# Kernel tuning notes

Measured on AMD Instinct MI355X. Metric: run time of the kernel, lower is better.

The kernel has to match this reference:

```python
import jax, jax.numpy as jnp
import numpy as np
import math

B, N, C, H = 32, 512, 768, 12
HD = C // H
KEEP_RATE = 0.7
SCALE = HD ** -0.5
BOUNDARY = math.ceil(KEEP_RATE * (N - 1))  # 358


def setup_inputs() -> dict:
    key = jax.random.key(0)
    k1, k2, k3, k4 = jax.random.split(key, 4)
    x = jax.random.normal(k1, (B, N, C), jnp.float32) * 0.02
    # prefix (left-aligned) key-padding mask: valid length per sample in [N//4, N]
    lengths = jax.random.randint(k2, (B,), N // 4, N + 1)
    key_mask = (jnp.arange(N)[None, :] < lengths[:, None])  # [B, N]
    attn_mask = jnp.broadcast_to(key_mask[:, None, :], (B, N, N)).astype(jnp.int32)
    w_qkv = jax.random.normal(k3, (C, 3 * C), jnp.float32) * (C ** -0.5)
    w_proj = jax.random.normal(k4, (C, C), jnp.float32) * (C ** -0.5)
    b_proj = jnp.zeros((C,), jnp.float32)
    return {"x": x, "attn_mask": attn_mask, "w_qkv": w_qkv, "w_proj": w_proj, "b_proj": b_proj}


def reference(x, attn_mask, w_qkv, w_proj, b_proj):
    # qkv projection and head split: [B,N,3C] -> [3,B,H,N,HD]
    qkv = (x @ w_qkv).reshape(B, N, 3, H, HD).transpose(2, 0, 3, 1, 4)
    q, k, v = qkv[0], qkv[1], qkv[2]
    attn = jnp.einsum('bhqd,bhkd->bhqk', q, k) * SCALE          # [B,H,N,N]
    mask4 = attn_mask[:, None, :, :]                            # broadcast over heads
    attn = jnp.where(mask4 == 0, jnp.float32(-1e9), attn)
    attn = jax.nn.softmax(attn, axis=-1)
    out = jnp.einsum('bhqk,bhkd->bhqd', attn, v)                # [B,H,N,HD]
    out = out.transpose(0, 2, 1, 3).reshape(B, N, C)
    out = out @ w_proj + b_proj

    # per-sample top-k token pruning based on CLS attention (keep_rate < 1)
    key_row = attn_mask[:, 0, 1:]                               # [B, N-1] key padding row
    cls_mean = attn[:, :, 0, 1:].mean(axis=1)                   # mean over heads, [B, N-1]
    valid = key_row != 0
    scores = jnp.where(valid, cls_mean, -jnp.inf)
    valid_count = valid.sum(axis=1)                             # [B]
    left = jnp.ceil(valid_count.astype(jnp.float32) * KEEP_RATE).astype(jnp.int32)
    _, top_idx = jax.lax.top_k(scores, BOUNDARY)                # sorted desc, [B, BOUNDARY]
    pos = jnp.arange(BOUNDARY)[None, :]
    # slots beyond per-sample left_tokens are padded with 1e9 (matches torch cat padding)
    idx = jnp.where(pos < left[:, None], top_idx.astype(jnp.float32), jnp.float32(1e9))
    index = jnp.broadcast_to(idx[:, :, None], (B, BOUNDARY, C))
    return (out, index, idx, BOUNDARY)
```

## Files before the change

### kernel.cpp

```cpp
#include <hip/hip_runtime.h>

#define Bb 32
#define Nn 512
#define Cc 768
#define Hh 12
#define HDd 64
#define BND 358
#define SCL 0.125f

typedef unsigned short u16;
typedef unsigned int u32;
typedef __attribute__((ext_vector_type(8))) short bf16x8;
typedef __attribute__((ext_vector_type(4))) float f32x4;
typedef __attribute__((ext_vector_type(4))) int i32x4;

__device__ __forceinline__ f32x4 MFMA16(bf16x8 a, bf16x8 b, f32x4 c) {
  return __builtin_amdgcn_mfma_f32_16x16x32_bf16(a, b, c, 0, 0, 0);
}

__device__ __forceinline__ u32 f2bf(float f) {
  u32 u = __builtin_bit_cast(u32, f);
  return (u + 0x7fffu + ((u >> 16) & 1u)) >> 16;
}
__device__ __forceinline__ u32 packbf2(float a, float b) { return f2bf(a) | (f2bf(b) << 16); }
__device__ __forceinline__ float bf2f(u16 h) { return __builtin_bit_cast(float, (u32)h << 16); }

__device__ __forceinline__ void async_copy16(void* lds, const void* g) {
  __builtin_amdgcn_global_load_lds((const __attribute__((address_space(1))) void*)g,
                                   (__attribute__((address_space(3))) void*)lds, 16, 0, 0);
}


__global__ __launch_bounds__(256) void k_convx(const float* __restrict__ x, u16* __restrict__ xb) {
  int gid = blockIdx.x * 256 + threadIdx.x;
  if (gid >= (Bb * Nn * Cc) / 4) return;
  float4 v = *(const float4*)&x[gid * 4];
  u32 p0 = packbf2(v.x, v.y), p1 = packbf2(v.z, v.w);
  uint2 st = {p0, p1};
  *(uint2*)&xb[gid * 4] = st;
}

__global__ __launch_bounds__(256) void k_transpose(const float* __restrict__ src, u16* __restrict__ dst,
                                                   int R, int Ccols) {
  __shared__ float tbuf[32][33];
  int c0 = blockIdx.x * 32, r0 = blockIdx.y * 32;
  int lx = threadIdx.x & 31, ly = threadIdx.x >> 5;
  #pragma unroll
  for (int rr = ly; rr < 32; rr += 8) tbuf[rr][lx] = src[(long)(r0 + rr) * Ccols + c0 + lx];
  __syncthreads();
  #pragma unroll
  for (int cc = ly; cc < 32; cc += 8) dst[(long)(c0 + cc) * R + r0 + lx] = (u16)f2bf(tbuf[lx][cc]);
}

__global__ __launch_bounds__(256) void k_lens(const int* __restrict__ mask, int* __restrict__ lens) {
  int b = blockIdx.x, t = threadIdx.x;
  __shared__ int red[256];
  red[t] = mask[(long)b * Nn * Nn + t] + mask[(long)b * Nn * Nn + t + 256];
  __syncthreads();
  for (int s = 128; s > 0; s >>= 1) {
    if (t < s) red[t] += red[t + s];
    __syncthreads();
  }
  if (t == 0) lens[b] = red[0];
}

template <int MODE, int SWAP>
__global__ __launch_bounds__(256) void k_gemm2(const u16* __restrict__ A, const u16* __restrict__ Bt,
                                               int nb0, u16* __restrict__ Qo, u16* __restrict__ Ko,
                                               u16* __restrict__ Vto, float* __restrict__ Co,
                                               const float* __restrict__ bias) {
  __shared__ u16 As[2][128 * 64];
  __shared__ u16 Bs[2][128 * 64];
  int m0 = blockIdx.x * 128;
  int nb = nb0 + blockIdx.y * 128;
  int t = threadIdx.x, lane = t & 63, wave = t >> 6;
  int wr = wave >> 1, wc = wave & 1;
  int qlane = lane & 15, g = lane >> 4;
  f32x4 acc[4][4] = {};

  auto stage = [&](int kt, int buf) {
    #pragma unroll
    for (int i = 0; i < 4; ++i) {
      int chunk = i * 256 + t;
      int row = chunk >> 3;
      int cp = (chunk & 7) << 4;
      int src = cp ^ ((row & 7) << 4);
      const u16* ga = A + (long)(m0 + row) * 768 + kt * 64 + (src >> 1);
      const u16* gb = Bt + (long)(nb + row) * 768 + kt * 64 + (src >> 1);
      async_copy16(&As[buf][(i * 256 + wave * 64) * 8], ga);
      async_copy16(&Bs[buf][(i * 256 + wave * 64) * 8], gb);
    }
  };

  auto compute = [&](int buf) {
    #pragma unroll
    for (int kk = 0; kk < 2; ++kk) {
      bf16x8 af[4], bf[4];
      #pragma unroll
      for (int x = 0; x < 4; ++x) {
        int ra = wr * 64 + x * 16 + qlane;
        int ca = (kk * 64 + g * 16) ^ ((ra & 7) << 4);
        af[x] = *(const bf16x8*)&As[buf][ra * 64 + (ca >> 1)];
        int rb = wc * 64 + x * 16 + qlane;
        int cb = (kk * 64 + g * 16) ^ ((rb & 7) << 4);
        bf[x] = *(const bf16x8*)&Bs[buf][rb * 64 + (cb >> 1)];
      }
      #pragma unroll
      for (int mi = 0; mi < 4; ++mi)
        #pragma unroll
        for (int ni = 0; ni < 4; ++ni)
          acc[mi][ni] = SWAP ? MFMA16(bf[ni], af[mi], acc[mi][ni])
                             : MFMA16(af[mi], bf[ni], acc[mi][ni]);
    }
  };

  stage(0, 0);
  __syncthreads();
  int cur = 0;
  for (int kt = 0; kt < 12; ++kt) {
    if (kt < 11) stage(kt + 1, cur ^ 1);
    compute(cur);
    __syncthreads();
    cur ^= 1;
  }

  if (MODE == 0 && SWAP == 1) {
    #pragma unroll
    for (int mi = 0; mi < 4; ++mi) {
      int m = m0 + wr * 64 + mi * 16 + qlane;
      int b = m >> 9, qi = m & 511;
      #pragma unroll
      for (int ni = 0; ni < 4; ++ni) {
        int nf = nb + wc * 64 + ni * 16 + g * 4;
        int which = nf >= 768;
        int rem = nf - which * 768;
        int hh = rem >> 6, d0 = rem & 63;
        u16* dst = (which ? Ko : Qo) + ((long)(b * Hh + hh) * Nn + qi) * HDd + d0;
        uint2 st = {packbf2(acc[mi][ni][0], acc[mi][ni][1]),
                    packbf2(acc[mi][ni][2], acc[mi][ni][3])};
        *(uint2*)dst = st;
      }
    }
  } else if (MODE == 0) {
    #pragma unroll
    for (int mi = 0; mi < 4; ++mi) {
      int m = m0 + wr * 64 + mi * 16 + g * 4;
      int b = m >> 9, qi = m & 511;
      #pragma unroll
      for (int ni = 0; ni < 4; ++ni) {
        int rem = nb + wc * 64 + ni * 16 + qlane - 1536;
        int hh = rem >> 6, d = rem & 63;
        u16* dst = Vto + ((long)(b * Hh + hh) * HDd + d) * Nn + qi;
        uint2 st = {packbf2(acc[mi][ni][0], acc[mi][ni][1]),
                    packbf2(acc[mi][ni][2], acc[mi][ni][3])};
        *(uint2*)dst = st;
      }
    }
  } else {
    #pragma unroll
    for (int mi = 0; mi < 4; ++mi) {
      #pragma unroll
      for (int ni = 0; ni < 4; ++ni) {
        int n = nb + wc * 64 + ni * 16 + qlane;
        float bv = bias[n];
        #pragma unroll
        for (int r = 0; r < 4; ++r) {
          int m = m0 + wr * 64 + mi * 16 + g * 4 + r;
          Co[(long)m * Cc + n] = acc[mi][ni][r] + bv;
        }
      }
    }
  }
}

__global__ __launch_bounds__(256) void k_attn(const u16* __restrict__ Q, const u16* __restrict__ K,
                                              const u16* __restrict__ Vt, const int* __restrict__ lens,
                                              u16* __restrict__ AO) {
  int wave = threadIdx.x >> 6, lane = threadIdx.x & 63;
  int bid = blockIdx.x;
  int half = bid & 1, h = (bid >> 1) % Hh, b = bid / (2 * Hh);
  int q0w = half * 256 + wave * 64;
  int qlane = lane & 15, g = lane >> 4;
  int len = lens[b];

  const u16* Qb = Q + (long)(b * Hh + h) * Nn * HDd;
  const u16* Kb = K + (long)(b * Hh + h) * Nn * HDd;
  const u16* Vb = Vt + (long)(b * Hh + h) * HDd * Nn;

  bf16x8 qf[4][2];
  #pragma unroll
  for (int t = 0; t < 4; ++t) {
    qf[t][0] = *(const bf16x8*)(Qb + (q0w + t * 16 + qlane) * HDd + g * 8);
    qf[t][1] = *(const bf16x8*)(Qb + (q0w + t * 16 + qlane) * HDd + 32 + g * 8);
  }

  f32x4 o[4][4] = {};
  float m[4] = {-1e30f, -1e30f, -1e30f, -1e30f};
  float l[4] = {0.f, 0.f, 0.f, 0.f};
  int srcA = qlane | ((2 * (g & 1)) << 4);
  int srcB = srcA | 16;
  bool hi = (g >> 1) != 0;

  #pragma unroll 1
  for (int c = 0; c < 8; ++c) {
    bf16x8 kf[4][2], vf[2][4];
    #pragma unroll
    for (int kt = 0; kt < 4; ++kt) {
      const u16* kp = Kb + ((c * 4 + kt) * 16 + qlane) * HDd + g * 8;
      kf[kt][0] = *(const bf16x8*)(kp);
      kf[kt][1] = *(const bf16x8*)(kp + 32);
    }
    #pragma unroll
    for (int c2 = 0; c2 < 2; ++c2)
      #pragma unroll
      for (int dt = 0; dt < 4; ++dt)
        vf[c2][dt] = *(const bf16x8*)(Vb + (dt * 16 + qlane) * Nn + c * 64 + c2 * 32 + g * 8);

    #pragma unroll
    for (int t = 0; t < 4; ++t) {
      f32x4 s[4];
      #pragma unroll
      for (int kt = 0; kt < 4; ++kt) {
        f32x4 a = {0.f, 0.f, 0.f, 0.f};
        a = MFMA16(kf[kt][0], qf[t][0], a);
        a = MFMA16(kf[kt][1], qf[t][1], a);
        s[kt] = a;
      }
      float pm = -1e30f;
      #pragma unroll
      for (int kt = 0; kt < 4; ++kt) {
        #pragma unroll
        for (int r = 0; r < 4; ++r) {
          int key = c * 64 + kt * 16 + g * 4 + r;
          float v = (key < len) ? s[kt][r] * SCL : -1e9f;
          s[kt][r] = v;
          pm = fmaxf(pm, v);
        }
      }
      pm = fmaxf(pm, __shfl_xor(pm, 16));
      pm = fmaxf(pm, __shfl_xor(pm, 32));
      if (!__all(pm <= m[t] + 8.f)) {
        float mn = fmaxf(m[t], pm);
        float sc = __expf(m[t] - mn);
        l[t] *= sc;
        #pragma unroll
        for (int dt = 0; dt < 4; ++dt) {
          o[t][dt][0] *= sc; o[t][dt][1] *= sc; o[t][dt][2] *= sc; o[t][dt][3] *= sc;
        }
        m[t] = mn;
      }
      u32 pk[4][2];
      #pragma unroll
      for (int kt = 0; kt < 4; ++kt) {
        float p0 = __expf(s[kt][0] - m[t]), p1 = __expf(s[kt][1] - m[t]);
        float p2 = __expf(s[kt][2] - m[t]), p3 = __expf(s[kt][3] - m[t]);
        l[t] += (p0 + p1) + (p2 + p3);
        pk[kt][0] = packbf2(p0, p1);
        pk[kt][1] = packbf2(p2, p3);
      }
      #pragma unroll
      for (int c2 = 0; c2 < 2; ++c2) {
        u32 a0 = (u32)__shfl((int)pk[2 * c2][0], srcA), b0 = (u32)__shfl((int)pk[2 * c2 + 1][0], srcA);
        u32 a1 = (u32)__shfl((int)pk[2 * c2][1], srcA), b1 = (u32)__shfl((int)pk[2 * c2 + 1][1], srcA);
        u32 a2 = (u32)__shfl((int)pk[2 * c2][0], srcB), b2 = (u32)__shfl((int)pk[2 * c2 + 1][0], srcB);
        u32 a3 = (u32)__shfl((int)pk[2 * c2][1], srcB), b3 = (u32)__shfl((int)pk[2 * c2 + 1][1], srcB);
        i32x4 w;
        w.x = (int)(hi ? b0 : a0);
        w.y = (int)(hi ? b1 : a1);
        w.z = (int)(hi ? b2 : a2);
        w.w = (int)(hi ? b3 : a3);
        bf16x8 pf = __builtin_bit_cast(bf16x8, w);
        #pragma unroll
        for (int dt = 0; dt < 4; ++dt) o[t][dt] = MFMA16(vf[c2][dt], pf, o[t][dt]);
      }
    }
  }

  #pragma unroll
  for (int t = 0; t < 4; ++t) {
    float ls = l[t];
    ls += __shfl_xor(ls, 16);
    ls += __shfl_xor(ls, 32);
    float inv = 1.f / ls;
    u16* outp = AO + ((long)(b * Nn + q0w + t * 16 + qlane) * Cc) + h * HDd;
    #pragma unroll
    for (int dt = 0; dt < 4; ++dt) {
      u32 lo = packbf2(o[t][dt][0] * inv, o[t][dt][1] * inv);
      u32 hi2 = packbf2(o[t][dt][2] * inv, o[t][dt][3] * inv);
      uint2 st = {lo, hi2};
      *(uint2*)(outp + dt * 16 + g * 4) = st;
    }
  }
}

__global__ __launch_bounds__(256) void k_sco_init(float* __restrict__ sco) {
  int gid = blockIdx.x * 256 + threadIdx.x;
  if (gid < Bb * 511) sco[gid] = 0.f;
}

__global__ __launch_bounds__(256) void k_cls(const u16* __restrict__ Q, const u16* __restrict__ K,
                                             const int* __restrict__ lens, float* __restrict__ scores) {
  int bh = blockIdx.x;
  int b = bh / Hh;
  int t = threadIdx.x;
  int len = lens[b];
  __shared__ float qrow[64];
  __shared__ float red[256];
  const u16* Qb = Q + (long)bh * Nn * HDd;
  const u16* Kb = K + (long)bh * Nn * HDd;
  if (t < 64) qrow[t] = bf2f(Qb[t]);
  __syncthreads();
  const bf16x8* kr0 = (const bf16x8*)(Kb + t * HDd);
  const bf16x8* kr1 = (const bf16x8*)(Kb + (t + 256) * HDd);
  float d0 = 0.f, d1 = 0.f;
  #pragma unroll
  for (int c8 = 0; c8 < 8; ++c8) {
    bf16x8 kv0 = kr0[c8], kv1 = kr1[c8];
    #pragma unroll
    for (int j = 0; j < 8; ++j) {
      float qv = qrow[c8 * 8 + j];
      d0 += qv * bf2f((u16)kv0[j]);
      d1 += qv * bf2f((u16)kv1[j]);
    }
  }
  float l0 = (t < len) ? d0 * SCL : -1e9f;
  float l1 = (t + 256 < len) ? d1 * SCL : -1e9f;
  red[t] = fmaxf(l0, l1);
  __syncthreads();
  for (int ss = 128; ss > 0; ss >>= 1) {
    if (t < ss) red[t] = fmaxf(red[t], red[t + ss]);
    __syncthreads();
  }
  float mx = red[0];
  __syncthreads();
  float e0 = __expf(l0 - mx), e1 = __expf(l1 - mx);
  red[t] = e0 + e1;
  __syncthreads();
  for (int ss = 128; ss > 0; ss >>= 1) {
    if (t < ss) red[t] += red[t + ss];
    __syncthreads();
  }
  float w = (1.f / 12.f) / red[0];
  if (t >= 1) atomicAdd(&scores[b * 511 + (t - 1)], e0 * w);
  atomicAdd(&scores[b * 511 + (t + 255)], e1 * w);
}

__device__ __forceinline__ bool sless(float sa, int ia, float sb, int ib) {
  return (sa > sb) || (sa == sb && ia < ib);
}

__global__ __launch_bounds__(256) void k_topk(const float* __restrict__ scores,
                                              const int* __restrict__ lens, float* __restrict__ dout) {
  int b = blockIdx.x, t = threadIdx.x;
  __shared__ float sc[512];
  __shared__ int id[512];
  float ninf = -__builtin_inff();
  int len = lens[b];
  for (int i = t; i < 512; i += 256) {
    sc[i] = (i < 511 && (i + 1) < len) ? scores[b * 511 + i] : ninf;
    id[i] = i;
  }
  for (int k = 2; k <= 512; k <<= 1) {
    for (int j = k >> 1; j > 0; j >>= 1) {
      __syncthreads();
      for (int i = t; i < 512; i += 256) {
        int ixj = i ^ j;
        if (ixj > i) {
          float si = sc[i], sj = sc[ixj];
          int ii = id[i], ij = id[ixj];
          bool up = ((i & k) == 0);
          bool dosw = up ? sless(sj, ij, si, ii) : sless(si, ii, sj, ij);
          if (dosw) {
            sc[i] = sj; sc[ixj] = si;
            id[i] = ij; id[ixj] = ii;
          }
        }
      }
    }
  }
  __syncthreads();
  int left = (int)ceilf((float)(len - 1) * 0.7f);
  const long OFF_IDX = (long)Bb * Nn * Cc + (long)Bb * BND * Cc;
  for (int p = t; p < BND; p += 256) {
    dout[OFF_IDX + (long)b * BND + p] = (p < left) ? (float)id[p] : 1e9f;
  }
  if (b == 0 && t == 0) dout[OFF_IDX + (long)Bb * BND] = (float)BND;
}

__global__ __launch_bounds__(256) void k_bcast(float* __restrict__ dout) {
  long gid = (long)blockIdx.x * 256 + threadIdx.x;
  const long total = (long)Bb * BND * (Cc / 4);
  if (gid >= total) return;
  long bp = gid / (Cc / 4);
  int c4 = (int)(gid % (Cc / 4));
  const long OFF_INDEX = (long)Bb * Nn * Cc;
  const long OFF_IDX = OFF_INDEX + (long)Bb * BND * Cc;
  float v = dout[OFF_IDX + bp];
  float4 f = {v, v, v, v};
  *(float4*)&dout[OFF_INDEX + bp * Cc + (long)c4 * 4] = f;
}

extern "C" void kernel_launch(void* const* d_in, const int* in_sizes, int n_in,
                              void* d_out, int out_size, void* d_ws, size_t ws_size,
                              hipStream_t stream) {
  const float* x = (const float*)d_in[0];
  const int* mask = (const int*)d_in[1];
  const float* wqkv = (const float*)d_in[2];
  const float* wproj = (const float*)d_in[3];
  const float* bproj = (const float*)d_in[4];
  float* out = (float*)d_out;

  char* ws = (char*)d_ws;
  u16* Qw  = (u16*)(ws);
  u16* Kw  = (u16*)(ws + 25165824L);
  u16* Vtw = (u16*)(ws + 50331648L);
  u16* XB  = (u16*)(ws + 75497472L);
  u16* AO  = XB;
  u16* WQT = (u16*)(ws + 100663296L);
  u16* WPT = (u16*)(ws + 104202240L);
  float* SCO = (float*)(ws + 105381888L);
  int* LEN = (int*)(ws + 105447424L);

  k_convx<<<12288, 256, 0, stream>>>(x, XB);
  k_transpose<<<dim3(72, 24), 256, 0, stream>>>(wqkv, WQT, 768, 2304);
  k_transpose<<<dim3(24, 24), 256, 0, stream>>>(wproj, WPT, 768, 768);
  k_lens<<<32, 256, 0, stream>>>(mask, LEN);
  k_sco_init<<<64, 256, 0, stream>>>(SCO);
  k_gemm2<0, 1><<<dim3(128, 12), 256, 0, stream>>>(XB, WQT, 0, Qw, Kw, nullptr, nullptr, nullptr);
  k_gemm2<0, 0><<<dim3(128, 6), 256, 0, stream>>>(XB, WQT, 1536, nullptr, nullptr, Vtw, nullptr, nullptr);
  k_attn<<<768, 256, 0, stream>>>(Qw, Kw, Vtw, LEN, AO);
  k_gemm2<1, 0><<<dim3(128, 6), 256, 0, stream>>>(AO, WPT, 0, nullptr, nullptr, nullptr, out, bproj);
  k_cls<<<384, 256, 0, stream>>>(Qw, Kw, LEN, SCO);
  k_topk<<<32, 256, 0, stream>>>(SCO, LEN, out);
  k_bcast<<<8592, 256, 0, stream>>>(out);
}
```

Baseline: 253.8 us.

## Skip masked key chunks, fold softmax scale and log2e into Q, use exp2

```diff
diff --git a/kernel.cpp b/kernel.cpp
--- a/kernel.cpp
+++ b/kernel.cpp
@@ -1,4 +1,5 @@
 #include <hip/hip_runtime.h>
+#include <hip/hip_bf16.h>
 
 #define Bb 32
 #define Nn 512
@@ -6,7 +7,7 @@
 #define Hh 12
 #define HDd 64
 #define BND 358
-#define SCL 0.125f
+#define QS 0.18033688f
 
 typedef unsigned short u16;
 typedef unsigned int u32;
@@ -23,6 +24,13 @@
   return (u + 0x7fffu + ((u >> 16) & 1u)) >> 16;
 }
 __device__ __forceinline__ u32 packbf2(float a, float b) { return f2bf(a) | (f2bf(b) << 16); }
+__device__ __forceinline__ u32 cvtpk2(float a, float b) {
+  float2 f2 = {a, b};
+  __hip_bfloat162 h = __float22bfloat162_rn(f2);
+  u32 r;
+  __builtin_memcpy(&r, &h, 4);
+  return r;
+}
 __device__ __forceinline__ float bf2f(u16 h) { return __builtin_bit_cast(float, (u32)h << 16); }
 
 __device__ __forceinline__ void async_copy16(void* lds, const void* g) {
@@ -136,8 +144,9 @@
         int rem = nf - which * 768;
         int hh = rem >> 6, d0 = rem & 63;
         u16* dst = (which ? Ko : Qo) + ((long)(b * Hh + hh) * Nn + qi) * HDd + d0;
-        uint2 st = {packbf2(acc[mi][ni][0], acc[mi][ni][1]),
-                    packbf2(acc[mi][ni][2], acc[mi][ni][3])};
+        float sc = which ? 1.f : QS;
+        uint2 st = {packbf2(acc[mi][ni][0] * sc, acc[mi][ni][1] * sc),
+                    packbf2(acc[mi][ni][2] * sc, acc[mi][ni][3] * sc)};
         *(uint2*)dst = st;
       }
     }
@@ -182,6 +191,7 @@
   int q0w = half * 256 + wave * 64;
   int qlane = lane & 15, g = lane >> 4;
   int len = lens[b];
+  int nc = (len + 63) >> 6;
 
   const u16* Qb = Q + (long)(b * Hh + h) * Nn * HDd;
   const u16* Kb = K + (long)(b * Hh + h) * Nn * HDd;
@@ -202,7 +212,7 @@
   bool hi = (g >> 1) != 0;
 
   #pragma unroll 1
-  for (int c = 0; c < 8; ++c) {
+  for (int c = 0; c < nc; ++c) {
     bf16x8 kf[4][2], vf[2][4];
     #pragma unroll
     for (int kt = 0; kt < 4; ++kt) {
@@ -215,6 +225,8 @@
       #pragma unroll
       for (int dt = 0; dt < 4; ++dt)
         vf[c2][dt] = *(const bf16x8*)(Vb + (dt * 16 + qlane) * Nn + c * 64 + c2 * 32 + g * 8);
+
+    bool boundary = (c * 64 + 64 > len);
 
     #pragma unroll
     for (int t = 0; t < 4; ++t) {
@@ -226,22 +238,26 @@
         a = MFMA16(kf[kt][1], qf[t][1], a);
         s[kt] = a;
       }
+      if (boundary) {
+        #pragma unroll
+        for (int kt = 0; kt < 4; ++kt)
+          #pragma unroll
+          for (int r = 0; r < 4; ++r) {
+            int key = c * 64 + kt * 16 + g * 4 + r;
+            if (key >= len) s[kt][r] = -1e9f;
+          }
+      }
       float pm = -1e30f;
       #pragma unroll
       for (int kt = 0; kt < 4; ++kt) {
-        #pragma unroll
-        for (int r = 0; r < 4; ++r) {
-          int key = c * 64 + kt * 16 + g * 4 + r;
-          float v = (key < len) ? s[kt][r] * SCL : -1e9f;
-          s[kt][r] = v;
-          pm = fmaxf(pm, v);
-        }
+        float m01 = fmaxf(s[kt][0], s[kt][1]);
+        pm = fmaxf(pm, fmaxf(m01, fmaxf(s[kt][2], s[kt][3])));
       }
       pm = fmaxf(pm, __shfl_xor(pm, 16));
       pm = fmaxf(pm, __shfl_xor(pm, 32));
-      if (!__all(pm <= m[t] + 8.f)) {
+      if (!__all(pm <= m[t] + 11.5f)) {
         float mn = fmaxf(m[t], pm);
-        float sc = __expf(m[t] - mn);
+        float sc = exp2f(m[t] - mn);
         l[t] *= sc;
         #pragma unroll
         for (int dt = 0; dt < 4; ++dt) {
@@ -252,11 +268,11 @@
       u32 pk[4][2];
       #pragma unroll
       for (int kt = 0; kt < 4; ++kt) {
-        float p0 = __expf(s[kt][0] - m[t]), p1 = __expf(s[kt][1] - m[t]);
-        float p2 = __expf(s[kt][2] - m[t]), p3 = __expf(s[kt][3] - m[t]);
+        float p0 = exp2f(s[kt][0] - m[t]), p1 = exp2f(s[kt][1] - m[t]);
+        float p2 = exp2f(s[kt][2] - m[t]), p3 = exp2f(s[kt][3] - m[t]);
         l[t] += (p0 + p1) + (p2 + p3);
-        pk[kt][0] = packbf2(p0, p1);
-        pk[kt][1] = packbf2(p2, p3);
+        pk[kt][0] = cvtpk2(p0, p1);
+        pk[kt][1] = cvtpk2(p2, p3);
       }
       #pragma unroll
       for (int c2 = 0; c2 < 2; ++c2) {
@@ -285,9 +301,8 @@
     u16* outp = AO + ((long)(b * Nn + q0w + t * 16 + qlane) * Cc) + h * HDd;
     #pragma unroll
     for (int dt = 0; dt < 4; ++dt) {
-      u32 lo = packbf2(o[t][dt][0] * inv, o[t][dt][1] * inv);
-      u32 hi2 = packbf2(o[t][dt][2] * inv, o[t][dt][3] * inv);
-      uint2 st = {lo, hi2};
+      uint2 st = {cvtpk2(o[t][dt][0] * inv, o[t][dt][1] * inv),
+                  cvtpk2(o[t][dt][2] * inv, o[t][dt][3] * inv)};
       *(uint2*)(outp + dt * 16 + g * 4) = st;
     }
   }
@@ -323,8 +338,8 @@
       d1 += qv * bf2f((u16)kv1[j]);
     }
   }
-  float l0 = (t < len) ? d0 * SCL : -1e9f;
-  float l1 = (t + 256 < len) ? d1 * SCL : -1e9f;
+  float l0 = (t < len) ? d0 : -1e9f;
+  float l1 = (t + 256 < len) ? d1 : -1e9f;
   red[t] = fmaxf(l0, l1);
   __syncthreads();
   for (int ss = 128; ss > 0; ss >>= 1) {
@@ -333,7 +348,7 @@
   }
   float mx = red[0];
   __syncthreads();
-  float e0 = __expf(l0 - mx), e1 = __expf(l1 - mx);
+  float e0 = exp2f(l0 - mx), e1 = exp2f(l1 - mx);
   red[t] = e0 + e1;
   __syncthreads();
   for (int ss = 128; ss > 0; ss >>= 1) {
```

New measurement: 257.1 us. Within noise of the previous version (+1.3%).
